# Optimization experiments

Hardware: AMD Instinct MI355X
Metric: run time of the kernel (lower is better)

The kernel has to match this reference:

```python
import jax, jax.numpy as jnp
import numpy as np

B, S, IN, H, E, OUT = 64, 2048, 256, 512, 256, 32000


def setup_inputs() -> dict:
    key = jax.random.key(0)
    ks = jax.random.split(key, 20)
    g = lambda k, shp, fan_in: jax.random.normal(k, shp, jnp.float32) / jnp.sqrt(jnp.float32(fan_in))
    return {
        "x": jax.random.normal(ks[0], (B, IN), jnp.float32),
        "hidden": jax.random.normal(ks[1], (B, H), jnp.float32),
        "encoder_outputs": jax.random.normal(ks[2], (B, S, H), jnp.float32),
        # attention params
        "W1_w": g(ks[3], (H, E), H), "W1_b": jnp.zeros((E,), jnp.float32),
        "W2_w": g(ks[4], (H, E), H),
        "v_w": g(ks[5], (E, 1), E),
        # GRU gate params (input to gates is concat(x, context): IN+H)
        "Wxr_w": g(ks[6], (IN + H, H), IN + H), "Wxr_b": jnp.zeros((H,), jnp.float32),
        "Whr_w": g(ks[7], (H, H), H),
        "Wxz_w": g(ks[8], (IN + H, H), IN + H), "Wxz_b": jnp.zeros((H,), jnp.float32),
        "Whz_w": g(ks[9], (H, H), H),
        "Wxh_w": g(ks[10], (IN + H, H), IN + H), "Wxh_b": jnp.zeros((H,), jnp.float32),
        "Whh_w": g(ks[11], (H, H), H),
        # output projection
        "Who_w": g(ks[12], (H, OUT), H), "Who_b": jnp.zeros((OUT,), jnp.float32),
    }


def reference(x, hidden, encoder_outputs,
              W1_w, W1_b, W2_w, v_w,
              Wxr_w, Wxr_b, Whr_w,
              Wxz_w, Wxz_b, Whz_w,
              Wxh_w, Wxh_b, Whh_w,
              Who_w, Who_b):
    # Bahdanau attention
    # energy: [B, S, E]
    energy = jnp.tanh(jnp.einsum("bsh,he->bse", encoder_outputs, W1_w) + W1_b
                      + (hidden @ W2_w)[:, None, :])
    scores = jnp.einsum("bse,eo->bs", energy, v_w)          # [B, S]
    attn_weights = jax.nn.softmax(scores, axis=1)            # [B, S]
    context = jnp.einsum("bs,bsh->bh", attn_weights, encoder_outputs)  # [B, H]

    x_context = jnp.concatenate([x, context], axis=-1)       # [B, IN+H]
    reset_gate = jax.nn.sigmoid(x_context @ Wxr_w + Wxr_b + hidden @ Whr_w)
    update_gate = jax.nn.sigmoid(x_context @ Wxz_w + Wxz_b + hidden @ Whz_w)
    h_tilde = jnp.tanh(x_context @ Wxh_w + Wxh_b + (reset_gate * hidden) @ Whh_w)
    new_hidden = update_gate * hidden + (1.0 - update_gate) * h_tilde
    output = new_hidden @ Who_w + Who_b                      # [B, OUT]
    return (output, new_hidden, attn_weights)
```

## Files before the change

kernel.cpp:

```cpp
#include <hip/hip_runtime.h>

#define BB 64
#define SS 2048
#define INDIM 256
#define HH 512
#define EE 256
#define OUTD 32000

typedef __attribute__((ext_vector_type(8))) short short8;
typedef __attribute__((ext_vector_type(4))) float floatx4;

#define LOG2E 1.4426950408889634f

__device__ __forceinline__ unsigned short f2bf(float f) {
  unsigned u = __float_as_uint(f);
  return (unsigned short)((u + 0x7FFFu + ((u >> 16) & 1u)) >> 16);
}
__device__ __forceinline__ unsigned pk2(float a, float b) {
  return (unsigned)f2bf(a) | ((unsigned)f2bf(b) << 16);
}
__device__ __forceinline__ float bf2f(unsigned short u) {
  return __uint_as_float((unsigned)u << 16);
}
__device__ __forceinline__ float fast_tanh(float x) {
  float e = __builtin_amdgcn_exp2f(x * 2.8853900817779268f);
  return 1.0f - 2.0f * __builtin_amdgcn_rcpf(e + 1.0f);
}
__device__ __forceinline__ float fast_sigmoid(float x) {
  float e = __builtin_amdgcn_exp2f(-x * LOG2E);
  return __builtin_amdgcn_rcpf(1.0f + e);
}

#define WS_W1T   0
#define WS_HBP   262144
#define WS_CTX   393216
#define WS_NHBF  524288
#define WS_Z     589824
#define WS_RH    720896
#define WS_GP    851968
#define WS_NP    3473408
#define WS_CTXP  4784128
#define WS_SUMP  21561344

__global__ void k_prep(const float* __restrict__ W1, unsigned short* __restrict__ W1t) {
  int idx = blockIdx.x * 256 + threadIdx.x;
  int k = idx >> 8, e = idx & 255;
  W1t[e * HH + k] = f2bf(W1[idx]);
}

__global__ __launch_bounds__(256) void k_hb(const float* __restrict__ hidden,
                                            const float* __restrict__ W2,
                                            const float* __restrict__ W1b,
                                            float* __restrict__ hbp) {
  int b0 = blockIdx.x * 4, seg = blockIdx.y, e = threadIdx.x;
  int h0 = seg * 256;
  float a0 = 0, a1 = 0, a2 = 0, a3 = 0;
  if (seg == 0) { a0 = a1 = a2 = a3 = W1b[e]; }
  for (int h = 0; h < 256; ++h) {
    float w = W2[(h0 + h) * EE + e];
    a0 += hidden[(b0 + 0) * HH + h0 + h] * w;
    a1 += hidden[(b0 + 1) * HH + h0 + h] * w;
    a2 += hidden[(b0 + 2) * HH + h0 + h] * w;
    a3 += hidden[(b0 + 3) * HH + h0 + h] * w;
  }
  float* o = hbp + (size_t)seg * BB * EE;
  o[(b0 + 0) * EE + e] = a0; o[(b0 + 1) * EE + e] = a1;
  o[(b0 + 2) * EE + e] = a2; o[(b0 + 3) * EE + e] = a3;
}

__global__ __launch_bounds__(256, 2) void k_scores(
    const float* __restrict__ enc, const unsigned short* __restrict__ W1t,
    const float* __restrict__ hbp, const float* __restrict__ vw,
    float* __restrict__ attn, float* __restrict__ ctxp, float* __restrict__ sump) {
  __shared__ unsigned short Afull[64 * 512];
  __shared__ float hb_s[EE], v_s[EE];
  __shared__ float red[4 * 64];
  __shared__ float wbuf[64];

  int tid = threadIdx.x;
  int m0 = blockIdx.x * 64;
  int b = blockIdx.x >> 5;
  int sloc = (blockIdx.x & 31) * 64;

  int lane = tid & 63, wn = tid >> 6;
  int l15 = lane & 15, quad = lane >> 4;

  int r0 = tid >> 3, j8 = tid & 7;
  const float* src0 = enc + (size_t)(m0 + r0) * HH + j8 * 4;
  const float* src1 = enc + (size_t)(m0 + 32 + r0) * HH + j8 * 4;
  float4 st0[16], st1[16];
#pragma unroll
  for (int i = 0; i < 16; ++i) st0[i] = *(const float4*)(src0 + i * 32);
#pragma unroll
  for (int i = 0; i < 16; ++i) st1[i] = *(const float4*)(src1 + i * 32);

  hb_s[tid] = hbp[b * EE + tid] + hbp[BB * EE + b * EE + tid];
  v_s[tid] = vw[tid];

#pragma unroll
  for (int i = 0; i < 16; ++i) {
    int sl = (j8 >> 1) + i * 4;
    {
      int r = r0;
      uint2 w; w.x = pk2(st0[i].x, st0[i].y); w.y = pk2(st0[i].z, st0[i].w);
      *(uint2*)((char*)Afull + r * 1024 + (sl ^ (r & 7)) * 16 + (j8 & 1) * 8) = w;
    }
    {
      int r = r0 + 32;
      uint2 w; w.x = pk2(st1[i].x, st1[i].y); w.y = pk2(st1[i].z, st1[i].w);
      *(uint2*)((char*)Afull + r * 1024 + (sl ^ (r & 7)) * 16 + (j8 & 1) * 8) = w;
    }
  }
  asm volatile("s_waitcnt lgkmcnt(0)" ::: "memory");
  __builtin_amdgcn_s_barrier();

  floatx4 acc[4][4];
#pragma unroll
  for (int i = 0; i < 4; ++i)
#pragma unroll
    for (int j = 0; j < 4; ++j) acc[i][j] = (floatx4)0.0f;

  const unsigned short* bbase = W1t + (size_t)(wn * 64) * HH;
#pragma unroll
  for (int kb = 0; kb < 16; ++kb) {
    short8 a[4];
#pragma unroll
    for (int i = 0; i < 4; ++i) {
      int r = i * 16 + l15;
      int ps = (kb * 4 + quad) ^ (l15 & 7);
      a[i] = *(const short8*)((const char*)Afull + r * 1024 + ps * 16);
    }
#pragma unroll
    for (int j = 0; j < 4; ++j) {
      short8 bfr = *(const short8*)(bbase + (size_t)(j * 16 + l15) * HH + kb * 32 + quad * 8);
#pragma unroll
      for (int i = 0; i < 4; ++i)
        acc[i][j] = __builtin_amdgcn_mfma_f32_16x16x32_bf16(a[i], bfr, acc[i][j], 0, 0, 0);
    }
  }
  __syncthreads();

#pragma unroll
  for (int i = 0; i < 4; ++i)
#pragma unroll
    for (int r = 0; r < 4; ++r) {
      float s = 0.0f;
#pragma unroll
      for (int j = 0; j < 4; ++j) {
        int e = wn * 64 + j * 16 + l15;
        s += fast_tanh(acc[i][j][r] + hb_s[e]) * v_s[e];
      }
#pragma unroll
      for (int off = 1; off < 16; off <<= 1) s += __shfl_xor(s, off, 64);
      if (l15 == 0) red[wn * 64 + i * 16 + quad * 4 + r] = s;
    }
  __syncthreads();
  if (tid < 64) {
    float sc = red[tid] + red[64 + tid] + red[128 + tid] + red[192 + tid];
    float e = __builtin_amdgcn_exp2f(sc * LOG2E);
    wbuf[tid] = e;
    attn[b * SS + sloc + tid] = e;
    float s = e;
#pragma unroll
    for (int off = 1; off < 64; off <<= 1) s += __shfl_xor(s, off, 64);
    if (tid == 0) sump[blockIdx.x] = s;
  }
  __syncthreads();

  float cacc[8];
#pragma unroll
  for (int j = 0; j < 8; ++j) cacc[j] = 0.0f;
#pragma unroll
  for (int rr = 0; rr < 16; ++rr) {
    int r = wn * 16 + rr;
    float w = wbuf[r];
    int ps = lane ^ (r & 7);
    short8 av = *(const short8*)((const char*)Afull + r * 1024 + ps * 16);
#pragma unroll
    for (int j = 0; j < 8; ++j) cacc[j] += w * bf2f((unsigned short)av[j]);
  }
  float4 c0, c1;
  c0.x = cacc[0]; c0.y = cacc[1]; c0.z = cacc[2]; c0.w = cacc[3];
  c1.x = cacc[4]; c1.y = cacc[5]; c1.z = cacc[6]; c1.w = cacc[7];
  float* cp = ctxp + ((size_t)blockIdx.x * 4 + wn) * HH + lane * 8;
  *(float4*)cp = c0;
  *(float4*)(cp + 4) = c1;
}

__global__ __launch_bounds__(512) void k_norm(float* __restrict__ attn,
                                              const float* __restrict__ ctxp,
                                              const float* __restrict__ sump,
                                              float* __restrict__ ctx) {
  int b = blockIdx.x, tid = threadIdx.x;
  float s = 0.0f;
#pragma unroll
  for (int t = 0; t < 32; ++t) s += sump[b * 32 + t];
  float inv = 1.0f / s;
#pragma unroll
  for (int i = 0; i < 4; ++i) attn[b * SS + tid + i * 512] *= inv;
  float c = 0.0f;
#pragma unroll 8
  for (int t = 0; t < 128; ++t) c += ctxp[(size_t)(b * 128 + t) * HH + tid];
  ctx[b * HH + tid] = c * inv;
}

__device__ __forceinline__ void part_seg(
    const float* __restrict__ Wx, const float* __restrict__ Wh,
    const float* __restrict__ x, const float* __restrict__ ctx,
    const float* __restrict__ hv, int seg, int b0, int h,
    float* __restrict__ outp) {
  const float* wseg;
  const float* a0; const float* a1; const float* a2; const float* a3;
  int vk0 = seg * 128;
  if (seg < 2) {
    wseg = Wx + (size_t)vk0 * HH;
    a0 = x + (b0 + 0) * INDIM + vk0;       a1 = x + (b0 + 1) * INDIM + vk0;
    a2 = x + (b0 + 2) * INDIM + vk0;       a3 = x + (b0 + 3) * INDIM + vk0;
  } else if (seg < 6) {
    wseg = Wx + (size_t)vk0 * HH;
    int off = vk0 - 256;
    a0 = ctx + (b0 + 0) * HH + off;        a1 = ctx + (b0 + 1) * HH + off;
    a2 = ctx + (b0 + 2) * HH + off;        a3 = ctx + (b0 + 3) * HH + off;
  } else {
    int off = vk0 - 768;
    wseg = Wh + (size_t)off * HH;
    a0 = hv + (b0 + 0) * HH + off;         a1 = hv + (b0 + 1) * HH + off;
    a2 = hv + (b0 + 2) * HH + off;         a3 = hv + (b0 + 3) * HH + off;
  }
  float s0 = 0, s1 = 0, s2 = 0, s3 = 0;
  for (int i = 0; i < 128; ++i) {
    float w = wseg[i * HH + h];
    s0 += a0[i] * w; s1 += a1[i] * w;
    s2 += a2[i] * w; s3 += a3[i] * w;
  }
  outp[(b0 + 0) * HH + h] = s0; outp[(b0 + 1) * HH + h] = s1;
  outp[(b0 + 2) * HH + h] = s2; outp[(b0 + 3) * HH + h] = s3;
}

__global__ __launch_bounds__(512) void k_gpart(
    const float* __restrict__ x, const float* __restrict__ ctx,
    const float* __restrict__ hidden,
    const float* __restrict__ Wxr, const float* __restrict__ Whr,
    const float* __restrict__ Wxz, const float* __restrict__ Whz,
    float* __restrict__ gp) {
  int b0 = blockIdx.x * 4, seg = blockIdx.y, sel = blockIdx.z, h = threadIdx.x;
  const float* Wx = sel ? Wxz : Wxr;
  const float* Wh = sel ? Whz : Whr;
  float* outp = gp + (size_t)(sel * 10 + seg) * BB * HH;
  part_seg(Wx, Wh, x, ctx, hidden, seg, b0, h, outp);
}

__global__ __launch_bounds__(512) void k_gred(
    const float* __restrict__ gp, const float* __restrict__ Wxrb,
    const float* __restrict__ Wxzb, const float* __restrict__ hidden,
    float* __restrict__ z_out, float* __restrict__ rh_out) {
  int b = blockIdx.x, h = threadIdx.x;
  float r = Wxrb[h], z = Wxzb[h];
#pragma unroll
  for (int s = 0; s < 10; ++s) {
    r += gp[((size_t)s * BB + b) * HH + h];
    z += gp[((size_t)(10 + s) * BB + b) * HH + h];
  }
  r = fast_sigmoid(r);
  z_out[b * HH + h] = fast_sigmoid(z);
  rh_out[b * HH + h] = r * hidden[b * HH + h];
}

__global__ __launch_bounds__(512) void k_npart(
    const float* __restrict__ x, const float* __restrict__ ctx,
    const float* __restrict__ rh,
    const float* __restrict__ Wxh, const float* __restrict__ Whh,
    float* __restrict__ np) {
  int b0 = blockIdx.x * 4, seg = blockIdx.y, h = threadIdx.x;
  float* outp = np + (size_t)seg * BB * HH;
  part_seg(Wxh, Whh, x, ctx, rh, seg, b0, h, outp);
}

__global__ __launch_bounds__(512) void k_nred(
    const float* __restrict__ np, const float* __restrict__ Wxhb,
    const float* __restrict__ z, const float* __restrict__ hidden,
    float* __restrict__ nh, unsigned short* __restrict__ nhbf) {
  int b = blockIdx.x, h = threadIdx.x;
  float a = Wxhb[h];
#pragma unroll
  for (int s = 0; s < 10; ++s) a += np[((size_t)s * BB + b) * HH + h];
  float ht = fast_tanh(a);
  float zz = z[b * HH + h];
  float val = zz * hidden[b * HH + h] + (1.0f - zz) * ht;
  nh[b * HH + h] = val;
  nhbf[b * HH + h] = f2bf(val);
}

__global__ __launch_bounds__(256) void k_out2(const unsigned short* __restrict__ nhbf,
                                              const float* __restrict__ Who,
                                              const float* __restrict__ Whob,
                                              float* __restrict__ out) {
  int tid = threadIdx.x;
  int lane = tid & 63, w = tid >> 6;
  int l15 = lane & 15, quad = lane >> 4;
  int n = blockIdx.x * 64 + w * 16 + l15;

  floatx4 acc[4];
#pragma unroll
  for (int i = 0; i < 4; ++i) acc[i] = (floatx4)0.0f;

#pragma unroll
  for (int kc = 0; kc < 16; ++kc) {
    int k0 = kc * 32;
    float bf[8];
    const float* bp = Who + (size_t)(k0 + quad * 8) * OUTD + n;
#pragma unroll
    for (int j = 0; j < 8; ++j) bf[j] = bp[(size_t)j * OUTD];
    union { unsigned u[4]; short8 v; } bu;
#pragma unroll
    for (int j = 0; j < 4; ++j) bu.u[j] = pk2(bf[2 * j], bf[2 * j + 1]);
#pragma unroll
    for (int i = 0; i < 4; ++i) {
      short8 af = *(const short8*)(nhbf + (i * 16 + l15) * HH + k0 + quad * 8);
      acc[i] = __builtin_amdgcn_mfma_f32_16x16x32_bf16(af, bu.v, acc[i], 0, 0, 0);
    }
  }
  float bias = Whob[n];
#pragma unroll
  for (int i = 0; i < 4; ++i)
#pragma unroll
    for (int r = 0; r < 4; ++r) {
      int m = i * 16 + quad * 4 + r;
      out[(size_t)m * OUTD + n] = acc[i][r] + bias;
    }
}

extern "C" void kernel_launch(void* const* d_in, const int* in_sizes, int n_in,
                              void* d_out, int out_size, void* d_ws, size_t ws_size,
                              hipStream_t stream) {
  const float* x    = (const float*)d_in[0];
  const float* hid  = (const float*)d_in[1];
  const float* enc  = (const float*)d_in[2];
  const float* W1w  = (const float*)d_in[3];
  const float* W1b  = (const float*)d_in[4];
  const float* W2w  = (const float*)d_in[5];
  const float* vw   = (const float*)d_in[6];
  const float* Wxr  = (const float*)d_in[7];
  const float* Wxrb = (const float*)d_in[8];
  const float* Whr  = (const float*)d_in[9];
  const float* Wxz  = (const float*)d_in[10];
  const float* Wxzb = (const float*)d_in[11];
  const float* Whz  = (const float*)d_in[12];
  const float* Wxh  = (const float*)d_in[13];
  const float* Wxhb = (const float*)d_in[14];
  const float* Whh  = (const float*)d_in[15];
  const float* Who  = (const float*)d_in[16];
  const float* Whob = (const float*)d_in[17];

  float* out  = (float*)d_out;
  float* nh   = out + (size_t)BB * OUTD;
  float* attn = nh + (size_t)BB * HH;

  char* ws = (char*)d_ws;
  unsigned short* W1t  = (unsigned short*)(ws + WS_W1T);
  float* hbp  = (float*)(ws + WS_HBP);
  float* ctx  = (float*)(ws + WS_CTX);
  unsigned short* nhbf = (unsigned short*)(ws + WS_NHBF);
  float* zg   = (float*)(ws + WS_Z);
  float* rh   = (float*)(ws + WS_RH);
  float* gp   = (float*)(ws + WS_GP);
  float* np   = (float*)(ws + WS_NP);
  float* ctxp = (float*)(ws + WS_CTXP);
  float* sump = (float*)(ws + WS_SUMP);

  k_prep<<<512, 256, 0, stream>>>(W1w, W1t);
  k_hb<<<dim3(16, 2), 256, 0, stream>>>(hid, W2w, W1b, hbp);
  k_scores<<<(BB * SS) / 64, 256, 0, stream>>>(enc, W1t, hbp, vw, attn, ctxp, sump);
  k_norm<<<BB, 512, 0, stream>>>(attn, ctxp, sump, ctx);
  k_gpart<<<dim3(16, 10, 2), 512, 0, stream>>>(x, ctx, hid, Wxr, Whr, Wxz, Whz, gp);
  k_gred<<<BB, 512, 0, stream>>>(gp, Wxrb, Wxzb, hid, zg, rh);
  k_npart<<<dim3(16, 10), 512, 0, stream>>>(x, ctx, rh, Wxh, Whh, np);
  k_nred<<<BB, 512, 0, stream>>>(np, Wxhb, zg, hid, nh, nhbf);
  k_out2<<<500, 256, 0, stream>>>(nhbf, Who, Whob, out);
}
```

Measured before the change: 571.7 us.

## Pre-convert encoder to swizzled bf16 and DMA into LDS; split GRU reductions finer

Adds a kernel that converts encoder_outputs to bf16 in a pre-swizzled layout in workspace, so the scores kernel can load its tile straight into LDS with global_load_lds instead of staging fp32 through registers and packing. The hidden projection and the GRU gate partial kernels are split into twice or four times as many K segments, giving more blocks at the cost of extra partial sums to reduce. The conversion adds a full fp32 read plus a bf16 write and read-back of the encoder tensor, which may outweigh the lower register pressure and the asynchronous load.

```diff
diff --git a/kernel.cpp b/kernel.cpp
--- a/kernel.cpp
+++ b/kernel.cpp
@@ -31,21 +31,48 @@
   return __builtin_amdgcn_rcpf(1.0f + e);
 }
 
+typedef __attribute__((address_space(1))) const void g1void;
+typedef __attribute__((address_space(3))) void l3void;
+__device__ __forceinline__ void dma16(const void* g, void* l) {
+  __builtin_amdgcn_global_load_lds((g1void*)g, (l3void*)l, 16, 0, 0);
+}
+
 #define WS_W1T   0
 #define WS_HBP   262144
-#define WS_CTX   393216
-#define WS_NHBF  524288
-#define WS_Z     589824
-#define WS_RH    720896
-#define WS_GP    851968
-#define WS_NP    3473408
-#define WS_CTXP  4784128
-#define WS_SUMP  21561344
+#define WS_CTX   786432
+#define WS_NHBF  917504
+#define WS_Z     983040
+#define WS_RH    1114112
+#define WS_GP    1245184
+#define WS_NP    6488064
+#define WS_CTXP  9109504
+#define WS_SUMP  25886720
+#define WS_ENCB  25894912
 
 __global__ void k_prep(const float* __restrict__ W1, unsigned short* __restrict__ W1t) {
   int idx = blockIdx.x * 256 + threadIdx.x;
   int k = idx >> 8, e = idx & 255;
   W1t[e * HH + k] = f2bf(W1[idx]);
+}
+
+__global__ __launch_bounds__(256) void k_conv(const float* __restrict__ enc,
+                                              unsigned short* __restrict__ encb) {
+  int tid = threadIdx.x;
+  int r_loc = tid >> 3, c0 = tid & 7;
+  int row = blockIdx.x * 32 + r_loc;
+  int rs = row & 7;
+  const float* src = enc + (size_t)row * HH;
+  unsigned short* dst = encb + (size_t)row * HH;
+#pragma unroll
+  for (int k = 0; k < 8; ++k) {
+    int c = c0 + k * 8;
+    float4 f0 = *(const float4*)(src + c * 8);
+    float4 f1 = *(const float4*)(src + c * 8 + 4);
+    uint4 w;
+    w.x = pk2(f0.x, f0.y); w.y = pk2(f0.z, f0.w);
+    w.z = pk2(f1.x, f1.y); w.w = pk2(f1.z, f1.w);
+    *(uint4*)(dst + (c ^ rs) * 8) = w;
+  }
 }
 
 __global__ __launch_bounds__(256) void k_hb(const float* __restrict__ hidden,
@@ -53,10 +80,10 @@
                                             const float* __restrict__ W1b,
                                             float* __restrict__ hbp) {
   int b0 = blockIdx.x * 4, seg = blockIdx.y, e = threadIdx.x;
-  int h0 = seg * 256;
+  int h0 = seg * 64;
   float a0 = 0, a1 = 0, a2 = 0, a3 = 0;
   if (seg == 0) { a0 = a1 = a2 = a3 = W1b[e]; }
-  for (int h = 0; h < 256; ++h) {
+  for (int h = 0; h < 64; ++h) {
     float w = W2[(h0 + h) * EE + e];
     a0 += hidden[(b0 + 0) * HH + h0 + h] * w;
     a1 += hidden[(b0 + 1) * HH + h0 + h] * w;
@@ -69,7 +96,7 @@
 }
 
 __global__ __launch_bounds__(256, 2) void k_scores(
-    const float* __restrict__ enc, const unsigned short* __restrict__ W1t,
+    const unsigned short* __restrict__ encb, const unsigned short* __restrict__ W1t,
     const float* __restrict__ hbp, const float* __restrict__ vw,
     float* __restrict__ attn, float* __restrict__ ctxp, float* __restrict__ sump) {
   __shared__ unsigned short Afull[64 * 512];
@@ -81,38 +108,22 @@
   int m0 = blockIdx.x * 64;
   int b = blockIdx.x >> 5;
   int sloc = (blockIdx.x & 31) * 64;
-
   int lane = tid & 63, wn = tid >> 6;
   int l15 = lane & 15, quad = lane >> 4;
 
-  int r0 = tid >> 3, j8 = tid & 7;
-  const float* src0 = enc + (size_t)(m0 + r0) * HH + j8 * 4;
-  const float* src1 = enc + (size_t)(m0 + 32 + r0) * HH + j8 * 4;
-  float4 st0[16], st1[16];
-#pragma unroll
-  for (int i = 0; i < 16; ++i) st0[i] = *(const float4*)(src0 + i * 32);
-#pragma unroll
-  for (int i = 0; i < 16; ++i) st1[i] = *(const float4*)(src1 + i * 32);
-
-  hb_s[tid] = hbp[b * EE + tid] + hbp[BB * EE + b * EE + tid];
-  v_s[tid] = vw[tid];
-
-#pragma unroll
-  for (int i = 0; i < 16; ++i) {
-    int sl = (j8 >> 1) + i * 4;
-    {
-      int r = r0;
-      uint2 w; w.x = pk2(st0[i].x, st0[i].y); w.y = pk2(st0[i].z, st0[i].w);
-      *(uint2*)((char*)Afull + r * 1024 + (sl ^ (r & 7)) * 16 + (j8 & 1) * 8) = w;
-    }
-    {
-      int r = r0 + 32;
-      uint2 w; w.x = pk2(st1[i].x, st1[i].y); w.y = pk2(st1[i].z, st1[i].w);
-      *(uint2*)((char*)Afull + r * 1024 + (sl ^ (r & 7)) * 16 + (j8 & 1) * 8) = w;
-    }
-  }
-  asm volatile("s_waitcnt lgkmcnt(0)" ::: "memory");
-  __builtin_amdgcn_s_barrier();
+#pragma unroll
+  for (int rr = 0; rr < 16; ++rr) {
+    int r = wn * 16 + rr;
+    dma16(encb + (size_t)(m0 + r) * HH + lane * 8, Afull + r * HH);
+  }
+  {
+    float hbv = 0.0f;
+#pragma unroll
+    for (int s = 0; s < 8; ++s) hbv += hbp[s * BB * EE + b * EE + tid];
+    hb_s[tid] = hbv;
+    v_s[tid] = vw[tid];
+  }
+  __syncthreads();
 
   floatx4 acc[4][4];
 #pragma unroll
@@ -127,8 +138,8 @@
 #pragma unroll
     for (int i = 0; i < 4; ++i) {
       int r = i * 16 + l15;
-      int ps = (kb * 4 + quad) ^ (l15 & 7);
-      a[i] = *(const short8*)((const char*)Afull + r * 1024 + ps * 16);
+      int pc = (kb * 4 + quad) ^ (l15 & 7);
+      a[i] = *(const short8*)(Afull + r * HH + pc * 8);
     }
 #pragma unroll
     for (int j = 0; j < 4; ++j) {
@@ -174,8 +185,8 @@
   for (int rr = 0; rr < 16; ++rr) {
     int r = wn * 16 + rr;
     float w = wbuf[r];
-    int ps = lane ^ (r & 7);
-    short8 av = *(const short8*)((const char*)Afull + r * 1024 + ps * 16);
+    int pc = lane ^ (r & 7);
+    short8 av = *(const short8*)(Afull + r * HH + pc * 8);
 #pragma unroll
     for (int j = 0; j < 8; ++j) cacc[j] += w * bf2f((unsigned short)av[j]);
   }
@@ -211,12 +222,12 @@
     float* __restrict__ outp) {
   const float* wseg;
   const float* a0; const float* a1; const float* a2; const float* a3;
-  int vk0 = seg * 128;
-  if (seg < 2) {
+  int vk0 = seg * 64;
+  if (seg < 4) {
     wseg = Wx + (size_t)vk0 * HH;
     a0 = x + (b0 + 0) * INDIM + vk0;       a1 = x + (b0 + 1) * INDIM + vk0;
     a2 = x + (b0 + 2) * INDIM + vk0;       a3 = x + (b0 + 3) * INDIM + vk0;
-  } else if (seg < 6) {
+  } else if (seg < 12) {
     wseg = Wx + (size_t)vk0 * HH;
     int off = vk0 - 256;
     a0 = ctx + (b0 + 0) * HH + off;        a1 = ctx + (b0 + 1) * HH + off;
@@ -228,7 +239,7 @@
     a2 = hv + (b0 + 2) * HH + off;         a3 = hv + (b0 + 3) * HH + off;
   }
   float s0 = 0, s1 = 0, s2 = 0, s3 = 0;
-  for (int i = 0; i < 128; ++i) {
+  for (int i = 0; i < 64; ++i) {
     float w = wseg[i * HH + h];
     s0 += a0[i] * w; s1 += a1[i] * w;
     s2 += a2[i] * w; s3 += a3[i] * w;
@@ -246,7 +257,7 @@
   int b0 = blockIdx.x * 4, seg = blockIdx.y, sel = blockIdx.z, h = threadIdx.x;
   const float* Wx = sel ? Wxz : Wxr;
   const float* Wh = sel ? Whz : Whr;
-  float* outp = gp + (size_t)(sel * 10 + seg) * BB * HH;
+  float* outp = gp + (size_t)(sel * 20 + seg) * BB * HH;
   part_seg(Wx, Wh, x, ctx, hidden, seg, b0, h, outp);
 }
 
@@ -257,9 +268,9 @@
   int b = blockIdx.x, h = threadIdx.x;
   float r = Wxrb[h], z = Wxzb[h];
 #pragma unroll
-  for (int s = 0; s < 10; ++s) {
+  for (int s = 0; s < 20; ++s) {
     r += gp[((size_t)s * BB + b) * HH + h];
-    z += gp[((size_t)(10 + s) * BB + b) * HH + h];
+    z += gp[((size_t)(20 + s) * BB + b) * HH + h];
   }
   r = fast_sigmoid(r);
   z_out[b * HH + h] = fast_sigmoid(z);
@@ -283,7 +294,7 @@
   int b = blockIdx.x, h = threadIdx.x;
   float a = Wxhb[h];
 #pragma unroll
-  for (int s = 0; s < 10; ++s) a += np[((size_t)s * BB + b) * HH + h];
+  for (int s = 0; s < 20; ++s) a += np[((size_t)s * BB + b) * HH + h];
   float ht = fast_tanh(a);
   float zz = z[b * HH + h];
   float val = zz * hidden[b * HH + h] + (1.0f - zz) * ht;
@@ -367,14 +378,16 @@
   float* np   = (float*)(ws + WS_NP);
   float* ctxp = (float*)(ws + WS_CTXP);
   float* sump = (float*)(ws + WS_SUMP);
+  unsigned short* encb = (unsigned short*)(ws + WS_ENCB);
 
   k_prep<<<512, 256, 0, stream>>>(W1w, W1t);
-  k_hb<<<dim3(16, 2), 256, 0, stream>>>(hid, W2w, W1b, hbp);
-  k_scores<<<(BB * SS) / 64, 256, 0, stream>>>(enc, W1t, hbp, vw, attn, ctxp, sump);
+  k_conv<<<(BB * SS) / 32, 256, 0, stream>>>(enc, encb);
+  k_hb<<<dim3(16, 8), 256, 0, stream>>>(hid, W2w, W1b, hbp);
+  k_scores<<<(BB * SS) / 64, 256, 0, stream>>>(encb, W1t, hbp, vw, attn, ctxp, sump);
   k_norm<<<BB, 512, 0, stream>>>(attn, ctxp, sump, ctx);
-  k_gpart<<<dim3(16, 10, 2), 512, 0, stream>>>(x, ctx, hid, Wxr, Whr, Wxz, Whz, gp);
+  k_gpart<<<dim3(16, 20, 2), 512, 0, stream>>>(x, ctx, hid, Wxr, Whr, Wxz, Whz, gp);
   k_gred<<<BB, 512, 0, stream>>>(gp, Wxrb, Wxzb, hid, zg, rh);
-  k_npart<<<dim3(16, 10), 512, 0, stream>>>(x, ctx, rh, Wxh, Whh, np);
+  k_npart<<<dim3(16, 20), 512, 0, stream>>>(x, ctx, rh, Wxh, Whh, np);
   k_nred<<<BB, 512, 0, stream>>>(np, Wxhb, zg, hid, nh, nhbf);
   k_out2<<<500, 256, 0, stream>>>(nhbf, Who, Whob, out);
 }
```

New measurement: 592.7 us. +3.7%, slower.
